# Optimization experiments

Hardware: AMD Instinct MI355X
Metric: run time of the kernel (lower is better)

## Reference

```python
import jax, jax.numpy as jnp
import numpy as np

D_IN = 1024
D_OUT = 1024

def setup_inputs() -> dict:
    key = jax.random.key(0)
    kx, kq, kk, kv = jax.random.split(key, 4)
    x = jax.random.normal(kx, (4, 2048, D_IN), dtype=jnp.float32)
    # torch Linear weights are [d_out, d_in]; store as [d_in, d_out] for x @ W
    s = 1.0 / np.sqrt(D_IN)
    Wq = jax.random.uniform(kq, (D_IN, D_OUT), jnp.float32, -s, s)
    Wk = jax.random.uniform(kk, (D_IN, D_OUT), jnp.float32, -s, s)
    Wv = jax.random.uniform(kv, (D_IN, D_OUT), jnp.float32, -s, s)
    return {"x": x, "Wq": Wq, "Wk": Wk, "Wv": Wv}

def reference(x, Wq, Wk, Wv):
    # x: [b, n, d_in]
    n = x.shape[1]
    q = jnp.einsum('bnd,de->bne', x, Wq)
    k = jnp.einsum('bnd,de->bne', x, Wk)
    v = jnp.einsum('bnd,de->bne', x, Wv)
    scores = jnp.einsum('bqe,bke->bqk', q, k)  # [b, n, n]
    causal = jnp.tril(jnp.ones((n, n), dtype=bool))  # True = keep
    scores = jnp.where(causal, scores, -jnp.inf)
    attn = jax.nn.softmax(scores / jnp.sqrt(jnp.float32(k.shape[-1])), axis=-1)
    # dropout p=0.0 -> identity
    return jnp.einsum('bqk,bke->bqe', attn, v)
```

## Files before the change

### kernel.cpp

```cpp
#include <hip/hip_runtime.h>
#include <hip/hip_bf16.h>
#include <stdint.h>

#define D_ 1024
#define NSEQ 2048

typedef __attribute__((ext_vector_type(8))) short bf16x8;
typedef __attribute__((ext_vector_type(4))) float f32x4;

static __device__ __forceinline__ unsigned short f2bf(float x) {
    union { __hip_bfloat16 h; unsigned short u; } cv;
    cv.h = __float2bfloat16(x);
    return cv.u;
}
static __device__ __forceinline__ float bf2f(unsigned short u) {
    union { float f; unsigned int i; } cv;
    cv.i = ((unsigned int)u) << 16;
    return cv.f;
}

static __device__ __forceinline__ void gload_lds16(const void* g, void* l) {
    __builtin_amdgcn_global_load_lds(
        (const __attribute__((address_space(1))) unsigned int*)(uintptr_t)g,
        (__attribute__((address_space(3))) unsigned int*)(uintptr_t)l, 16, 0, 0);
}

__global__ __launch_bounds__(256) void cvt_x(const float* __restrict__ x,
                                             __hip_bfloat16* __restrict__ xb) {
    int i = blockIdx.x * 256 + threadIdx.x;
    float4 v = reinterpret_cast<const float4*>(x)[i];
    ushort4 o;
    o.x = f2bf(v.x); o.y = f2bf(v.y); o.z = f2bf(v.z); o.w = f2bf(v.w);
    reinterpret_cast<ushort4*>(xb)[i] = o;
}

__global__ __launch_bounds__(256) void wt_kernel(const float* __restrict__ Wq,
                                                 const float* __restrict__ Wk,
                                                 const float* __restrict__ Wv,
                                                 __hip_bfloat16* __restrict__ Wt) {
    const float* W = (blockIdx.z == 0) ? Wq : (blockIdx.z == 1) ? Wk : Wv;
    unsigned short* O = (unsigned short*)(Wt + (size_t)blockIdx.z * D_ * D_);
    __shared__ float tile[32][33];
    int r0 = blockIdx.y * 32, c0 = blockIdx.x * 32;
    int t = threadIdx.x;
    int r = t >> 3, c4 = (t & 7) * 4;
    float4 v = *reinterpret_cast<const float4*>(&W[(size_t)(r0 + r) * D_ + c0 + c4]);
    tile[r][c4 + 0] = v.x; tile[r][c4 + 1] = v.y;
    tile[r][c4 + 2] = v.z; tile[r][c4 + 3] = v.w;
    __syncthreads();
    int er = t >> 3, dc = (t & 7) * 4;
    ushort4 pk;
    pk.x = f2bf(tile[dc + 0][er]); pk.y = f2bf(tile[dc + 1][er]);
    pk.z = f2bf(tile[dc + 2][er]); pk.w = f2bf(tile[dc + 3][er]);
    *reinterpret_cast<ushort4*>(&O[(size_t)(c0 + er) * D_ + r0 + dc]) = pk;
}

template <int MODE>
__global__ __launch_bounds__(256) void gemm128(const __hip_bfloat16* __restrict__ A, int lda,
                                               const __hip_bfloat16* __restrict__ Bt, int ldb,
                                               void* __restrict__ o0, void* __restrict__ o1,
                                               void* __restrict__ o2,
                                               const float2* __restrict__ rl) {
    int bx, by, bz;
    if (MODE == 0) {
        bx = blockIdx.x; by = blockIdx.y; bz = 0;
    } else if (MODE == 2) {
        const int fid = blockIdx.x;
        bz = fid & 3;
        const int t = fid >> 2;
        bx = (int)((sqrtf(8.0f * t + 1.0f) - 1.0f) * 0.5f);
        while ((bx + 1) * (bx + 2) / 2 <= t) ++bx;
        while (bx * (bx + 1) / 2 > t) --bx;
        by = t - bx * (bx + 1) / 2;
    } else {
        const int fid = blockIdx.x;
        const int bxr = fid & 15;
        bx = (fid & 256) ? 15 - bxr : bxr;
        bz = (fid >> 4) & 3;
        by = fid >> 6;
    }

    const __hip_bfloat16* Ab = A;
    const __hip_bfloat16* Bb = Bt;
    int Kdim = 1024;
    if (MODE == 2) { Ab += (size_t)bz * NSEQ * lda; Bb += (size_t)bz * NSEQ * ldb; }
    if (MODE == 3) { Ab += (size_t)bz * NSEQ * lda; Bb += (size_t)bz * D_ * ldb; Kdim = (bx + 1) * 128; }

    const int m0 = bx * 128, n0 = by * 128;

    __shared__ __hip_bfloat16 As[128 * 64];
    __shared__ __hip_bfloat16 Bs[128 * 64];

    const int tid = threadIdx.x;
    const int lane = tid & 63, wid = tid >> 6;
    const int wm = wid >> 1, wn = wid & 1;
    const int lr = lane & 15, lk = lane >> 4;

    const __hip_bfloat16* asrc[4];
    const __hip_bfloat16* bsrc[4];
#pragma unroll
    for (int r = 0; r < 4; ++r) {
        const int chunk = r * 256 + tid;
        const int row = chunk >> 3, slot = chunk & 7;
        const int col = ((slot ^ (row & 7)) * 8);
        asrc[r] = Ab + (size_t)(m0 + row) * lda + col;
        bsrc[r] = Bb + (size_t)(n0 + row) * ldb + col;
    }

    const int sw = lr & 7;
    const int slotA0 = (lk ^ sw) * 16, slotA1 = ((4 + lk) ^ sw) * 16;

    f32x4 acc[4][4] = {};

    for (int k0 = 0; k0 < Kdim; k0 += 64) {
#pragma unroll
        for (int r = 0; r < 4; ++r) {
            gload_lds16(asrc[r], (char*)As + r * 4096 + wid * 1024);
            gload_lds16(bsrc[r], (char*)Bs + r * 4096 + wid * 1024);
            asrc[r] += 64; bsrc[r] += 64;
        }
        __syncthreads();

        bf16x8 af0[4], bf0[4], af1[4], bf1[4];
#pragma unroll
        for (int m = 0; m < 4; ++m) {
            const int ra = (wm * 64 + m * 16 + lr) * 128;
            const int rb = (wn * 64 + m * 16 + lr) * 128;
            af0[m] = *reinterpret_cast<const bf16x8*>((const char*)As + ra + slotA0);
            af1[m] = *reinterpret_cast<const bf16x8*>((const char*)As + ra + slotA1);
            bf0[m] = *reinterpret_cast<const bf16x8*>((const char*)Bs + rb + slotA0);
            bf1[m] = *reinterpret_cast<const bf16x8*>((const char*)Bs + rb + slotA1);
        }
#pragma unroll
        for (int m = 0; m < 4; ++m)
#pragma unroll
            for (int n = 0; n < 4; ++n)
                acc[m][n] = __builtin_amdgcn_mfma_f32_16x16x32_bf16(af0[m], bf0[n], acc[m][n], 0, 0, 0);
#pragma unroll
        for (int m = 0; m < 4; ++m)
#pragma unroll
            for (int n = 0; n < 4; ++n)
                acc[m][n] = __builtin_amdgcn_mfma_f32_16x16x32_bf16(af1[m], bf1[n], acc[m][n], 0, 0, 0);
        __syncthreads();
    }

    if (MODE == 0) {
#pragma unroll
        for (int m = 0; m < 4; ++m)
#pragma unroll
            for (int n = 0; n < 4; ++n) {
                const int rbase = m0 + wm * 64 + m * 16 + lk * 4;
                const int cbase = n0 + wn * 64 + n * 16 + lr;
                const int seg = cbase >> 10, e = cbase & 1023;
                if (seg < 2) {
                    unsigned short* C = (unsigned short*)(seg == 0 ? o0 : o1);
#pragma unroll
                    for (int j = 0; j < 4; ++j)
                        C[(size_t)(rbase + j) * D_ + e] = f2bf(acc[m][n][j]);
                } else {
                    unsigned short* Vt = (unsigned short*)o2;
                    const int b = rbase >> 11, nq = rbase & 2047;
                    ushort4 pk;
                    pk.x = f2bf(acc[m][n][0]); pk.y = f2bf(acc[m][n][1]);
                    pk.z = f2bf(acc[m][n][2]); pk.w = f2bf(acc[m][n][3]);
                    *reinterpret_cast<ushort4*>(&Vt[(((size_t)b << 10) + e) * NSEQ + nq]) = pk;
                }
            }
    } else if (MODE == 2) {
        unsigned short* S = (unsigned short*)o0 + (size_t)bz * NSEQ * NSEQ;
#pragma unroll
        for (int m = 0; m < 4; ++m)
#pragma unroll
            for (int n = 0; n < 4; ++n) {
                const int rbase = m0 + wm * 64 + m * 16 + lk * 4;
                const int cbase = n0 + wn * 64 + n * 16 + lr;
#pragma unroll
                for (int j = 0; j < 4; ++j) {
                    float s = acc[m][n][j] * 0.03125f;
                    if (cbase > rbase + j) s = -1e30f;
                    acc[m][n][j] = s;
                    S[(size_t)(rbase + j) * NSEQ + cbase] = f2bf(s);
                }
            }
        float* Pm = (float*)o1;
        float* Pl = (float*)o2;
        const int pcol = by * 2 + wn;
#pragma unroll
        for (int m = 0; m < 4; ++m)
#pragma unroll
            for (int j = 0; j < 4; ++j) {
                float mx = fmaxf(fmaxf(acc[m][0][j], acc[m][1][j]),
                                 fmaxf(acc[m][2][j], acc[m][3][j]));
#pragma unroll
                for (int w = 1; w < 16; w <<= 1) mx = fmaxf(mx, __shfl_xor(mx, w, 64));
                float sm = __expf(acc[m][0][j] - mx) + __expf(acc[m][1][j] - mx) +
                           __expf(acc[m][2][j] - mx) + __expf(acc[m][3][j] - mx);
#pragma unroll
                for (int w = 1; w < 16; w <<= 1) sm += __shfl_xor(sm, w, 64);
                if (lr == 0) {
                    const int row = bz * NSEQ + m0 + wm * 64 + m * 16 + lk * 4 + j;
                    Pm[row * 32 + pcol] = mx;
                    Pl[row * 32 + pcol] = sm;
                }
            }
    } else {
        float* O = (float*)o0 + (size_t)bz * NSEQ * D_;
#pragma unroll
        for (int m = 0; m < 4; ++m)
#pragma unroll
            for (int n = 0; n < 4; ++n) {
                const int rbase = m0 + wm * 64 + m * 16 + lk * 4;
                const int cbase = n0 + wn * 64 + n * 16 + lr;
#pragma unroll
                for (int j = 0; j < 4; ++j)
                    O[(size_t)(rbase + j) * D_ + cbase] =
                        acc[m][n][j] * rl[bz * NSEQ + rbase + j].y;
            }
    }
}

__global__ __launch_bounds__(256) void softmax_finish(unsigned short* __restrict__ S,
                                                      const float* __restrict__ Pm,
                                                      const float* __restrict__ Pl,
                                                      float2* __restrict__ rl) {
    const int lane = threadIdx.x & 63;
    const int row = blockIdx.x * 4 + (threadIdx.x >> 6);
    const int q = row & 2047;
    const int nb = (q >> 7) + 1;
    const int nc = nb * 2;

    float mb = (lane < nc) ? Pm[row * 32 + lane] : -3e38f;
    float m = mb;
#pragma unroll
    for (int off = 32; off > 0; off >>= 1) m = fmaxf(m, __shfl_xor(m, off, 64));
    float lb = (lane < nc) ? Pl[row * 32 + lane] * __expf(mb - m) : 0.f;
#pragma unroll
    for (int off = 32; off > 0; off >>= 1) lb += __shfl_xor(lb, off, 64);
    if (lane == 0) rl[row] = make_float2(m, 1.0f / lb);

    unsigned short* srow = S + (size_t)row * NSEQ;
    const int L = nb << 7;
    for (int k = lane * 8; k < L; k += 512) {
        ushort4 a = *reinterpret_cast<const ushort4*>(srow + k);
        ushort4 b = *reinterpret_cast<const ushort4*>(srow + k + 4);
        ushort4 pa, pb;
        pa.x = f2bf(__expf(bf2f(a.x) - m)); pa.y = f2bf(__expf(bf2f(a.y) - m));
        pa.z = f2bf(__expf(bf2f(a.z) - m)); pa.w = f2bf(__expf(bf2f(a.w) - m));
        pb.x = f2bf(__expf(bf2f(b.x) - m)); pb.y = f2bf(__expf(bf2f(b.y) - m));
        pb.z = f2bf(__expf(bf2f(b.z) - m)); pb.w = f2bf(__expf(bf2f(b.w) - m));
        *reinterpret_cast<ushort4*>(srow + k)     = pa;
        *reinterpret_cast<ushort4*>(srow + k + 4) = pb;
    }
}

extern "C" void kernel_launch(void* const* d_in, const int* in_sizes, int n_in,
                              void* d_out, int out_size, void* d_ws, size_t ws_size,
                              hipStream_t stream) {
    const float* x  = (const float*)d_in[0];
    const float* Wq = (const float*)d_in[1];
    const float* Wk = (const float*)d_in[2];
    const float* Wv = (const float*)d_in[3];

    char* ws = (char*)d_ws;
    unsigned short* S    = (unsigned short*)(ws);
    __hip_bfloat16* Xb   = (__hip_bfloat16*)(ws + 67108864);
    __hip_bfloat16* Q    = (__hip_bfloat16*)(ws + 83886080);
    __hip_bfloat16* K    = (__hip_bfloat16*)(ws + 100663296);
    __hip_bfloat16* Vt   = (__hip_bfloat16*)(ws + 117440512);
    __hip_bfloat16* Wt   = (__hip_bfloat16*)(ws + 134217728);
    float*  Pm = (float*)(ws + 67108864);
    float*  Pl = (float*)(ws + 68157440);
    float2* rl = (float2*)(ws + 69206016);

    cvt_x<<<8192, 256, 0, stream>>>(x, Xb);
    wt_kernel<<<dim3(32, 32, 3), 256, 0, stream>>>(Wq, Wk, Wv, Wt);

    gemm128<0><<<dim3(64, 24, 1), 256, 0, stream>>>(Xb, 1024, Wt, 1024, Q, K, Vt, nullptr);

    gemm128<2><<<dim3(544), 256, 0, stream>>>(Q, 1024, K, 1024, S, Pm, Pl, nullptr);
    softmax_finish<<<2048, 256, 0, stream>>>(S, Pm, Pl, rl);
    gemm128<3><<<dim3(512), 256, 0, stream>>>((const __hip_bfloat16*)S, 2048, Vt, 2048,
                                              d_out, nullptr, nullptr, rl);
}
```

Baseline: 169.7 us.

## Replace QKV projection GEMM with 256x128 triple-buffered 512-thread kernel

Adds a dedicated QKV projection kernel that uses 256x128 tiles with 8 waves, a three-stage LDS ring filled by direct global-to-LDS loads, and explicit vmcnt waits so loads for tile t+2 overlap compute on tile t. It also raises wave priority around the MFMA block. The aim is to hide global-load latency and reuse each B tile across more rows in the largest projection GEMM. In exchange it needs 144 KB of dynamic LDS per block, which limits occupancy, and the launch grid is halved.

```diff
diff --git a/kernel.cpp b/kernel.cpp
--- a/kernel.cpp
+++ b/kernel.cpp
@@ -55,6 +55,112 @@
     *reinterpret_cast<ushort4*>(&O[(size_t)(c0 + er) * D_ + r0 + dc]) = pk;
 }
 
+__global__ __launch_bounds__(512, 2) void gemm_qkv(
+    const __hip_bfloat16* __restrict__ A,
+    const __hip_bfloat16* __restrict__ Bt,
+    void* __restrict__ q_out, void* __restrict__ k_out, void* __restrict__ vt_out) {
+    constexpr int NT = 16;
+    extern __shared__ char lds[];
+
+    const int m0 = blockIdx.x * 256, n0 = blockIdx.y * 128;
+    const int tid = threadIdx.x, lane = tid & 63, wid = tid >> 6;
+    const int wm = wid >> 1, wn = wid & 1;
+    const int lr = lane & 15, lk = lane >> 4;
+
+    const __hip_bfloat16* Apan = A + (size_t)m0 * 1024;
+    const __hip_bfloat16* Bpan = Bt + (size_t)n0 * 1024;
+
+    const __hip_bfloat16* asrc[4];
+    const __hip_bfloat16* bsrc[2];
+#pragma unroll
+    for (int r = 0; r < 4; ++r) {
+        const int c = (wid * 4 + r) * 64 + lane;
+        const int row = c >> 3, slot = c & 7;
+        asrc[r] = Apan + (size_t)row * 1024 + (slot ^ (row & 7)) * 8;
+    }
+#pragma unroll
+    for (int r = 0; r < 2; ++r) {
+        const int c = (wid * 2 + r) * 64 + lane;
+        const int row = c >> 3, slot = c & 7;
+        bsrc[r] = Bpan + (size_t)row * 1024 + (slot ^ (row & 7)) * 8;
+    }
+
+    auto stage = [&](int s) {
+        char* base = lds + (s % 3) * 49152;
+#pragma unroll
+        for (int r = 0; r < 4; ++r) {
+            gload_lds16(asrc[r], base + (wid * 4 + r) * 1024);
+            asrc[r] += 64;
+        }
+#pragma unroll
+        for (int r = 0; r < 2; ++r) {
+            gload_lds16(bsrc[r], base + 32768 + (wid * 2 + r) * 1024);
+            bsrc[r] += 64;
+        }
+    };
+
+    const int sw = lr & 7;
+    const int slot0 = (lk ^ sw) * 16, slot1 = ((4 + lk) ^ sw) * 16;
+
+    f32x4 acc[4][4] = {};
+
+    stage(0); stage(1);
+
+    for (int t = 0; t < NT; ++t) {
+        if (t >= NT - 1) asm volatile("s_waitcnt vmcnt(0)" ::: "memory");
+        else             asm volatile("s_waitcnt vmcnt(6)" ::: "memory");
+        __builtin_amdgcn_s_barrier();
+        if (t + 2 < NT) stage(t + 2);
+
+        const char* Ab = lds + (t % 3) * 49152;
+        const char* Bb = Ab + 32768;
+        bf16x8 af0[4], af1[4], bf0[4], bf1[4];
+#pragma unroll
+        for (int m = 0; m < 4; ++m) {
+            const int ra = (wm * 64 + m * 16 + lr) * 128;
+            const int rb = (wn * 64 + m * 16 + lr) * 128;
+            af0[m] = *reinterpret_cast<const bf16x8*>(Ab + ra + slot0);
+            af1[m] = *reinterpret_cast<const bf16x8*>(Ab + ra + slot1);
+            bf0[m] = *reinterpret_cast<const bf16x8*>(Bb + rb + slot0);
+            bf1[m] = *reinterpret_cast<const bf16x8*>(Bb + rb + slot1);
+        }
+        __builtin_amdgcn_s_setprio(1);
+#pragma unroll
+        for (int m = 0; m < 4; ++m)
+#pragma unroll
+            for (int n = 0; n < 4; ++n)
+                acc[m][n] = __builtin_amdgcn_mfma_f32_16x16x32_bf16(af0[m], bf0[n], acc[m][n], 0, 0, 0);
+#pragma unroll
+        for (int m = 0; m < 4; ++m)
+#pragma unroll
+            for (int n = 0; n < 4; ++n)
+                acc[m][n] = __builtin_amdgcn_mfma_f32_16x16x32_bf16(af1[m], bf1[n], acc[m][n], 0, 0, 0);
+        __builtin_amdgcn_s_setprio(0);
+    }
+
+#pragma unroll
+    for (int m = 0; m < 4; ++m)
+#pragma unroll
+        for (int n = 0; n < 4; ++n) {
+            const int rbase = m0 + wm * 64 + m * 16 + lk * 4;
+            const int cbase = n0 + wn * 64 + n * 16 + lr;
+            const int seg = cbase >> 10, e = cbase & 1023;
+            if (seg < 2) {
+                unsigned short* C = (unsigned short*)(seg == 0 ? q_out : k_out);
+#pragma unroll
+                for (int j = 0; j < 4; ++j)
+                    C[(size_t)(rbase + j) * D_ + e] = f2bf(acc[m][n][j]);
+            } else {
+                unsigned short* Vt = (unsigned short*)vt_out;
+                const int b = rbase >> 11, nq = rbase & 2047;
+                ushort4 pk;
+                pk.x = f2bf(acc[m][n][0]); pk.y = f2bf(acc[m][n][1]);
+                pk.z = f2bf(acc[m][n][2]); pk.w = f2bf(acc[m][n][3]);
+                *reinterpret_cast<ushort4*>(&Vt[(((size_t)b << 10) + e) * NSEQ + nq]) = pk;
+            }
+        }
+}
+
 template <int MODE>
 __global__ __launch_bounds__(256) void gemm128(const __hip_bfloat16* __restrict__ A, int lda,
                                                const __hip_bfloat16* __restrict__ Bt, int ldb,
@@ -62,9 +168,7 @@
                                                void* __restrict__ o2,
                                                const float2* __restrict__ rl) {
     int bx, by, bz;
-    if (MODE == 0) {
-        bx = blockIdx.x; by = blockIdx.y; bz = 0;
-    } else if (MODE == 2) {
+    if (MODE == 2) {
         const int fid = blockIdx.x;
         bz = fid & 3;
         const int t = fid >> 2;
@@ -144,29 +248,7 @@
         __syncthreads();
     }
 
-    if (MODE == 0) {
-#pragma unroll
-        for (int m = 0; m < 4; ++m)
-#pragma unroll
-            for (int n = 0; n < 4; ++n) {
-                const int rbase = m0 + wm * 64 + m * 16 + lk * 4;
-                const int cbase = n0 + wn * 64 + n * 16 + lr;
-                const int seg = cbase >> 10, e = cbase & 1023;
-                if (seg < 2) {
-                    unsigned short* C = (unsigned short*)(seg == 0 ? o0 : o1);
-#pragma unroll
-                    for (int j = 0; j < 4; ++j)
-                        C[(size_t)(rbase + j) * D_ + e] = f2bf(acc[m][n][j]);
-                } else {
-                    unsigned short* Vt = (unsigned short*)o2;
-                    const int b = rbase >> 11, nq = rbase & 2047;
-                    ushort4 pk;
-                    pk.x = f2bf(acc[m][n][0]); pk.y = f2bf(acc[m][n][1]);
-                    pk.z = f2bf(acc[m][n][2]); pk.w = f2bf(acc[m][n][3]);
-                    *reinterpret_cast<ushort4*>(&Vt[(((size_t)b << 10) + e) * NSEQ + nq]) = pk;
-                }
-            }
-    } else if (MODE == 2) {
+    if (MODE == 2) {
         unsigned short* S = (unsigned short*)o0 + (size_t)bz * NSEQ * NSEQ;
 #pragma unroll
         for (int m = 0; m < 4; ++m)
@@ -275,7 +357,7 @@
     cvt_x<<<8192, 256, 0, stream>>>(x, Xb);
     wt_kernel<<<dim3(32, 32, 3), 256, 0, stream>>>(Wq, Wk, Wv, Wt);
 
-    gemm128<0><<<dim3(64, 24, 1), 256, 0, stream>>>(Xb, 1024, Wt, 1024, Q, K, Vt, nullptr);
+    gemm_qkv<<<dim3(32, 24), 512, 147456, stream>>>(Xb, Wt, Q, K, Vt);
 
     gemm128<2><<<dim3(544), 256, 0, stream>>>(Q, 1024, K, 1024, S, Pm, Pl, nullptr);
     softmax_finish<<<2048, 256, 0, stream>>>(S, Pm, Pl, rl);
```

Result: no change. 171.5 us (+1.0%).
